# Performance work log

Measured on AMD Instinct MI355X. Metric: run time of the kernel, lower is better.

The kernel has to match this reference:

```python
import jax, jax.numpy as jnp
import numpy as np
import math

DIM = 2048
NUM_HEADS = 16
HEAD_DIM = 128
SEQ = 2048
BATCH = 2
THETA = 10000.0


def _rope_freqs(seq_len, head_dim, theta=THETA):
    half = head_dim // 2
    inv = 1.0 / (theta ** (np.arange(0, half, dtype=np.float32) / half))
    t = np.arange(seq_len, dtype=np.float32)
    ang = np.outer(t, inv)  # [S, half]
    return jnp.asarray(np.cos(ang)), jnp.asarray(np.sin(ang))


def setup_inputs() -> dict:
    key = jax.random.key(0)
    ks = jax.random.split(key, 5)
    s = 1.0 / math.sqrt(DIM)
    cos, sin = _rope_freqs(SEQ, HEAD_DIM)
    return {
        "x": jax.random.normal(ks[0], (BATCH, SEQ, DIM), dtype=jnp.float32),
        "wq": jax.random.normal(ks[1], (DIM, NUM_HEADS * HEAD_DIM), dtype=jnp.float32) * s,
        "wk": jax.random.normal(ks[2], (DIM, NUM_HEADS * HEAD_DIM), dtype=jnp.float32) * s,
        "wv": jax.random.normal(ks[3], (DIM, NUM_HEADS * HEAD_DIM), dtype=jnp.float32) * s,
        "wo": jax.random.normal(ks[4], (NUM_HEADS * HEAD_DIM, DIM), dtype=jnp.float32) * s,
        "freqs_cos": cos,
        "freqs_sin": sin,
    }


def _apply_rope(x, cos, sin):
    # x: [B, S, H, Hd]; cos/sin: [S, Hd//2]
    B, S, H, Hd = x.shape
    xr = x.astype(jnp.float32).reshape(B, S, H, Hd // 2, 2)
    x0, x1 = xr[..., 0], xr[..., 1]
    c = cos[:S][None, :, None, :]
    sn = sin[:S][None, :, None, :]
    o0 = x0 * c - x1 * sn
    o1 = x0 * sn + x1 * c
    return jnp.stack([o0, o1], axis=-1).reshape(B, S, H, Hd)


def reference(x, wq, wk, wv, wo, freqs_cos, freqs_sin):
    B, S, D = x.shape
    H, Hd = NUM_HEADS, HEAD_DIM
    q = (x @ wq).reshape(B, S, H, Hd)
    k = (x @ wk).reshape(B, S, H, Hd)
    v = (x @ wv).reshape(B, S, H, Hd)
    q = _apply_rope(q, freqs_cos, freqs_sin)
    k = _apply_rope(k, freqs_cos, freqs_sin)
    # [B, H, S, S] causal attention scores
    scores = jnp.einsum("bqhd,bkhd->bhqk", q, k) / math.sqrt(Hd)
    causal = jnp.tril(jnp.ones((S, S), dtype=bool))
    scores = jnp.where(causal[None, None], scores, -jnp.inf)
    probs = jax.nn.softmax(scores.astype(jnp.float32), axis=-1)
    o = jnp.einsum("bhqk,bkhd->bqhd", probs, v).reshape(B, S, H * Hd)
    return o @ wo
```

## Files before the change

kernel.cpp:

```cpp
#include <hip/hip_runtime.h>
#include <hip/hip_bf16.h>

typedef __bf16 bf16;
typedef __attribute__((ext_vector_type(8))) __bf16 bf16x8;
typedef __attribute__((ext_vector_type(4))) __bf16 bf16x4;
typedef __attribute__((ext_vector_type(4))) float  f32x4;

typedef const void __attribute__((address_space(1)))* gas_t;
typedef void __attribute__((address_space(3)))* las_t;

__device__ __forceinline__ void gload16(const void* g, void* l) {
  __builtin_amdgcn_global_load_lds((gas_t)g, (las_t)l, 16, 0, 0);
}
__device__ __forceinline__ f32x4 mfma16(bf16x8 a, bf16x8 b, f32x4 c) {
  return __builtin_amdgcn_mfma_f32_16x16x32_bf16(a, b, c, 0, 0, 0);
}

constexpr int SEQL = 2048;
constexpr int DM   = 2048;
constexpr int HD   = 128;
constexpr int MR   = 4096;

__global__ __launch_bounds__(256) void cvt_x(const float* __restrict__ x,
                                             bf16* __restrict__ xb) {
  const size_t i = ((size_t)blockIdx.x * 256 + threadIdx.x) * 4;
  const f32x4 v = *reinterpret_cast<const f32x4*>(x + i);
  bf16x4 o;
  #pragma unroll
  for (int j = 0; j < 4; ++j) o[j] = (bf16)v[j];
  *reinterpret_cast<bf16x4*>(xb + i) = o;
}

__global__ __launch_bounds__(256) void transpose_w(
    const float* __restrict__ w0, const float* __restrict__ w1,
    const float* __restrict__ w2, const float* __restrict__ w3,
    bf16* __restrict__ wqkvt, bf16* __restrict__ wot) {
  const int z = blockIdx.z;
  const float* src = (z == 0) ? w0 : (z == 1) ? w1 : (z == 2) ? w2 : w3;
  bf16* dst = (z < 3) ? (wqkvt + (size_t)z * DM * DM) : wot;
  __shared__ float tile[32][33];
  const int tx = threadIdx.x, ty = threadIdx.y;
  const int x0 = blockIdx.x * 32, y0 = blockIdx.y * 32;
  #pragma unroll
  for (int i = 0; i < 4; ++i)
    tile[ty + 8 * i][tx] = src[(size_t)(y0 + ty + 8 * i) * DM + x0 + tx];
  __syncthreads();
  #pragma unroll
  for (int i = 0; i < 4; ++i)
    dst[(size_t)(x0 + ty + 8 * i) * DM + y0 + tx] = (bf16)tile[tx][ty + 8 * i];
}

__global__ __launch_bounds__(256) void rope_k(bf16* __restrict__ Q,
                                              bf16* __restrict__ Kk,
                                              const float* __restrict__ fc,
                                              const float* __restrict__ fs) {
  bf16* X = blockIdx.y ? Kk : Q;
  const size_t tid = (size_t)blockIdx.x * 256 + threadIdx.x;
  const size_t e0 = tid * 8;
  const int col = (int)(e0 & (DM - 1));
  const int row = (int)(e0 >> 11);
  const int s   = row & (SEQL - 1);
  const int p0  = (col & (HD - 1)) >> 1;
  bf16x8 v = *reinterpret_cast<bf16x8*>(X + e0);
  const f32x4 c  = *reinterpret_cast<const f32x4*>(fc + (size_t)s * 64 + p0);
  const f32x4 sn = *reinterpret_cast<const f32x4*>(fs + (size_t)s * 64 + p0);
  #pragma unroll
  for (int j = 0; j < 4; ++j) {
    const float x0 = (float)v[2 * j], x1 = (float)v[2 * j + 1];
    v[2 * j]     = (bf16)(x0 * c[j] - x1 * sn[j]);
    v[2 * j + 1] = (bf16)(x0 * sn[j] + x1 * c[j]);
  }
  *reinterpret_cast<bf16x8*>(X + e0) = v;
}

template <bool MULTI, bool OUTF32>
__global__ __launch_bounds__(256) void gemm_bt(
    const bf16* __restrict__ A, const bf16* __restrict__ Bt,
    bf16* __restrict__ Cb, float* __restrict__ Cf,
    const int M, const int N, const int K) {
  const int t = threadIdx.x;
  const int wid = t >> 6, lane = t & 63, lo = lane & 15, hi = lane >> 4;
  const int m0 = blockIdx.y * 128, n0 = blockIdx.x * 128;
  const bf16* Bt_ = Bt;
  bf16* Cb_ = Cb;
  if (MULTI) {
    const size_t z = blockIdx.z;
    Bt_ += z * (size_t)N * K;
    Cb_ += z * (size_t)M * N;
  }
  __shared__ bf16 As[128 * 32];
  __shared__ bf16 Bs[128 * 32];
  const int wr = wid >> 1, wc = wid & 1;
  const f32x4 zero4 = {0.f, 0.f, 0.f, 0.f};
  f32x4 acc[4][4];
  #pragma unroll
  for (int i = 0; i < 4; ++i)
    #pragma unroll
    for (int j = 0; j < 4; ++j) acc[i][j] = zero4;

  const int r_a = t >> 2;
  const int ul  = ((t & 3) ^ (r_a & 3)) * 8;
  const bf16* gA0 = A   + (size_t)(m0 + r_a) * K + ul;
  const bf16* gB0 = Bt_ + (size_t)(n0 + r_a) * K + ul;
  char* lA = (char*)As + wid * 1024;
  char* lB = (char*)Bs + wid * 1024;

  const int ru = (hi ^ (lo & 3)) * 8;

  for (int k0 = 0; k0 < K; k0 += 32) {
    gload16(gA0 + k0, lA);
    gload16(gA0 + (size_t)64 * K + k0, lA + 4096);
    gload16(gB0 + k0, lB);
    gload16(gB0 + (size_t)64 * K + k0, lB + 4096);
    __syncthreads();
    bf16x8 af[4], bb[4];
    #pragma unroll
    for (int i = 0; i < 4; ++i)
      af[i] = *reinterpret_cast<const bf16x8*>(As + (wr * 64 + i * 16 + lo) * 32 + ru);
    #pragma unroll
    for (int i = 0; i < 4; ++i)
      bb[i] = *reinterpret_cast<const bf16x8*>(Bs + (wc * 64 + i * 16 + lo) * 32 + ru);
    #pragma unroll
    for (int mi = 0; mi < 4; ++mi)
      #pragma unroll
      for (int ni = 0; ni < 4; ++ni)
        acc[mi][ni] = mfma16(af[mi], bb[ni], acc[mi][ni]);
    __syncthreads();
  }
  #pragma unroll
  for (int mi = 0; mi < 4; ++mi)
    #pragma unroll
    for (int ni = 0; ni < 4; ++ni)
      #pragma unroll
      for (int r = 0; r < 4; ++r) {
        const size_t row = m0 + wr * 64 + mi * 16 + hi * 4 + r;
        const size_t col = n0 + wc * 64 + ni * 16 + lo;
        if (OUTF32) Cf[row * N + col] = acc[mi][ni][r];
        else        Cb_[row * N + col] = (bf16)acc[mi][ni][r];
      }
}

__global__ __launch_bounds__(256) void flash_fwd(
    const bf16* __restrict__ Qg, const bf16* __restrict__ Kg,
    const bf16* __restrict__ Vg, bf16* __restrict__ Og) {
  const int t = threadIdx.x;
  const int wid = t >> 6, lane = t & 63, lo = lane & 15, hi = lane >> 4;
  const int q0 = blockIdx.x * 64;
  const int h  = blockIdx.y;
  const int b  = blockIdx.z;

  __shared__ bf16 Ks[64 * 128];
  __shared__ bf16 Vt[128 * 64];
  __shared__ bf16 Ps[4][16 * 64];

  const size_t hoff = (size_t)b * SEQL * DM + (size_t)h * HD;

  bf16x8 qf[4];
  {
    const bf16* qrow = Qg + hoff + (size_t)(q0 + wid * 16 + lo) * DM;
    #pragma unroll
    for (int kc = 0; kc < 4; ++kc)
      qf[kc] = *reinterpret_cast<const bf16x8*>(qrow + kc * 32 + hi * 8);
  }

  const f32x4 zero4 = {0.f, 0.f, 0.f, 0.f};
  f32x4 acc[8];
  #pragma unroll
  for (int i = 0; i < 8; ++i) acc[i] = zero4;
  float m_r[4], l_r[4];
  #pragma unroll
  for (int r = 0; r < 4; ++r) { m_r[r] = -1e30f; l_r[r] = 0.f; }

  const int ntiles = q0 / 64 + 1;
  const float scale = 0.08838834764831845f;

  const int krow = t >> 4;
  const int kul  = ((t & 15) ^ krow) * 8;
  const int vd0  = (t & 31) * 4;
  const int vg   = t >> 5;

  for (int it = 0; it < ntiles; ++it) {
    const int kv0 = it * 64;
    {
      const bf16* gK = Kg + hoff + (size_t)(kv0 + krow) * DM + kul;
      char* lK = (char*)Ks + wid * 1024;
      #pragma unroll
      for (int j = 0; j < 4; ++j)
        gload16(gK + (size_t)j * 16 * DM, lK + j * 4096);
    }
    {
      const bf16* gV = Vg + hoff + (size_t)kv0 * DM + vd0;
      bf16x4 ld[8];
      #pragma unroll
      for (int e = 0; e < 8; ++e)
        ld[e] = *reinterpret_cast<const bf16x4*>(gV + (size_t)(vg * 8 + e) * DM);
      #pragma unroll
      for (int c = 0; c < 4; ++c) {
        const int d = vd0 + c;
        const int sw = (d ^ (d >> 3)) & 7;
        bf16x8 pk;
        #pragma unroll
        for (int e = 0; e < 8; ++e) pk[e] = ld[e][c];
        *reinterpret_cast<bf16x8*>(Vt + d * 64 + ((vg ^ sw) * 8)) = pk;
      }
    }
    __syncthreads();

    f32x4 s[4];
    #pragma unroll
    for (int nf = 0; nf < 4; ++nf) s[nf] = zero4;
    #pragma unroll
    for (int nf = 0; nf < 4; ++nf) {
      const bf16* krp = Ks + (nf * 16 + lo) * 128;
      #pragma unroll
      for (int kc = 0; kc < 4; ++kc) {
        const bf16x8 kb = *reinterpret_cast<const bf16x8*>(krp + (((kc * 4 + hi) ^ lo) * 8));
        s[nf] = mfma16(qf[kc], kb, s[nf]);
      }
    }
    const bool boundary = (kv0 == q0);
    #pragma unroll
    for (int nf = 0; nf < 4; ++nf)
      #pragma unroll
      for (int r = 0; r < 4; ++r) {
        float v = s[nf][r] * scale;
        if (boundary && (nf * 16 + lo > wid * 16 + hi * 4 + r)) v = -1e30f;
        s[nf][r] = v;
      }
    float fctr[4];
    #pragma unroll
    for (int r = 0; r < 4; ++r) {
      float mx = fmaxf(fmaxf(s[0][r], s[1][r]), fmaxf(s[2][r], s[3][r]));
      #pragma unroll
      for (int msk = 1; msk < 16; msk <<= 1) mx = fmaxf(mx, __shfl_xor(mx, msk, 64));
      const float mnew = fmaxf(m_r[r], mx);
      fctr[r] = __expf(m_r[r] - mnew);
      m_r[r] = mnew;
      float sum = 0.f;
      #pragma unroll
      for (int nf = 0; nf < 4; ++nf) {
        const float p = __expf(s[nf][r] - mnew);
        s[nf][r] = p;
        sum += p;
      }
      l_r[r] = l_r[r] * fctr[r] + sum;
    }
    #pragma unroll
    for (int i = 0; i < 8; ++i)
      #pragma unroll
      for (int r = 0; r < 4; ++r) acc[i][r] *= fctr[r];
    bf16* myP = Ps[wid];
    #pragma unroll
    for (int nf = 0; nf < 4; ++nf)
      #pragma unroll
      for (int r = 0; r < 4; ++r) {
        const int row = hi * 4 + r;
        const int col = nf * 16 + lo;
        myP[row * 64 + (((col >> 3) ^ (row & 7)) * 8) + (col & 7)] = (bf16)s[nf][r];
      }
    bf16x8 pa[2];
    #pragma unroll
    for (int kc = 0; kc < 2; ++kc)
      pa[kc] = *reinterpret_cast<const bf16x8*>(myP + lo * 64 + (((kc * 4 + hi) ^ (lo & 7)) * 8));
    #pragma unroll
    for (int nf = 0; nf < 8; ++nf) {
      const int d = nf * 16 + lo;
      const int sw = (d ^ (d >> 3)) & 7;
      const bf16* vrp = Vt + d * 64;
      #pragma unroll
      for (int kc = 0; kc < 2; ++kc) {
        const bf16x8 bv = *reinterpret_cast<const bf16x8*>(vrp + (((kc * 4 + hi) ^ sw) * 8));
        acc[nf] = mfma16(pa[kc], bv, acc[nf]);
      }
    }
    __syncthreads();
  }

  #pragma unroll
  for (int r = 0; r < 4; ++r) {
    float l = l_r[r];
    #pragma unroll
    for (int msk = 1; msk < 16; msk <<= 1) l += __shfl_xor(l, msk, 64);
    l_r[r] = 1.f / l;
  }
  #pragma unroll
  for (int nf = 0; nf < 8; ++nf)
    #pragma unroll
    for (int r = 0; r < 4; ++r) {
      const size_t row = q0 + wid * 16 + hi * 4 + r;
      Og[hoff + row * DM + nf * 16 + lo] = (bf16)(acc[nf][r] * l_r[r]);
    }
}

extern "C" void kernel_launch(void* const* d_in, const int* in_sizes, int n_in,
                              void* d_out, int out_size, void* d_ws, size_t ws_size,
                              hipStream_t stream) {
  const float* x  = (const float*)d_in[0];
  const float* wq = (const float*)d_in[1];
  const float* wk = (const float*)d_in[2];
  const float* wv = (const float*)d_in[3];
  const float* wo = (const float*)d_in[4];
  const float* fc = (const float*)d_in[5];
  const float* fs = (const float*)d_in[6];
  float* out = (float*)d_out;

  char* ws = (char*)d_ws;
  bf16* xb    = (bf16*)ws;
  bf16* wqkvt = (bf16*)(ws + (16ull << 20));
  bf16* wot   = (bf16*)(ws + (40ull << 20));
  bf16* qkv   = (bf16*)(ws + (48ull << 20));
  bf16* Qb = qkv;
  bf16* Kb = qkv + (size_t)MR * DM;
  bf16* Vb = qkv + 2 * (size_t)MR * DM;

  cvt_x<<<8192, 256, 0, stream>>>(x, xb);
  transpose_w<<<dim3(64, 64, 4), dim3(32, 8), 0, stream>>>(wq, wk, wv, wo, wqkvt, wot);
  gemm_bt<true, false><<<dim3(16, 32, 3), 256, 0, stream>>>(xb, wqkvt, qkv, nullptr, MR, DM, DM);
  rope_k<<<dim3(4096, 2), 256, 0, stream>>>(Qb, Kb, fc, fs);
  flash_fwd<<<dim3(32, 16, 2), 256, 0, stream>>>(Qb, Kb, Vb, xb );
  gemm_bt<false, true><<<dim3(16, 32), 256, 0, stream>>>(xb, wot, nullptr, out, MR, DM, DM);
}
```

Measured before the change: 506.4 us.

## Pair causal query tiles per block and streamline flash-attention softmax

Each flash-attention block now handles two query tiles (i and 31-i), halving the grid so every block does equal causal work. The QK^T MFMA operands are swapped so each lane owns one query row, which turns the row max and sum reductions into two cross-lane shuffles. The softmax uses exp2 with a folded log2 scale and skips rescaling the accumulator when no row max in the wave grows. The P store to shared memory is vectorised. The cost is a grid of 512 blocks instead of 1024, which may lower occupancy and latency hiding on a chip with many CUs.

```diff
diff --git a/kernel.cpp b/kernel.cpp
--- a/kernel.cpp
+++ b/kernel.cpp
@@ -145,7 +145,6 @@
     const bf16* __restrict__ Vg, bf16* __restrict__ Og) {
   const int t = threadIdx.x;
   const int wid = t >> 6, lane = t & 63, lo = lane & 15, hi = lane >> 4;
-  const int q0 = blockIdx.x * 64;
   const int h  = blockIdx.y;
   const int b  = blockIdx.z;
 
@@ -154,142 +153,154 @@
   __shared__ bf16 Ps[4][16 * 64];
 
   const size_t hoff = (size_t)b * SEQL * DM + (size_t)h * HD;
-
-  bf16x8 qf[4];
-  {
-    const bf16* qrow = Qg + hoff + (size_t)(q0 + wid * 16 + lo) * DM;
-    #pragma unroll
-    for (int kc = 0; kc < 4; ++kc)
-      qf[kc] = *reinterpret_cast<const bf16x8*>(qrow + kc * 32 + hi * 8);
-  }
-
-  const f32x4 zero4 = {0.f, 0.f, 0.f, 0.f};
-  f32x4 acc[8];
-  #pragma unroll
-  for (int i = 0; i < 8; ++i) acc[i] = zero4;
-  float m_r[4], l_r[4];
-  #pragma unroll
-  for (int r = 0; r < 4; ++r) { m_r[r] = -1e30f; l_r[r] = 0.f; }
-
-  const int ntiles = q0 / 64 + 1;
-  const float scale = 0.08838834764831845f;
+  const float SCALE_LOG2 = 0.12751743f;
 
   const int krow = t >> 4;
   const int kul  = ((t & 15) ^ krow) * 8;
   const int vd0  = (t & 31) * 4;
   const int vg   = t >> 5;
-
-  for (int it = 0; it < ntiles; ++it) {
-    const int kv0 = it * 64;
+  char* myP = (char*)(Ps[wid]);
+  const f32x4 zero4 = {0.f, 0.f, 0.f, 0.f};
+
+  #pragma unroll 1
+  for (int pass = 0; pass < 2; ++pass) {
+    const int q0 = (pass ? (31 - (int)blockIdx.x) : (int)blockIdx.x) * 64;
+
+    bf16x8 qf[4];
     {
-      const bf16* gK = Kg + hoff + (size_t)(kv0 + krow) * DM + kul;
-      char* lK = (char*)Ks + wid * 1024;
-      #pragma unroll
-      for (int j = 0; j < 4; ++j)
-        gload16(gK + (size_t)j * 16 * DM, lK + j * 4096);
+      const bf16* qrow = Qg + hoff + (size_t)(q0 + wid * 16 + lo) * DM;
+      #pragma unroll
+      for (int kc = 0; kc < 4; ++kc)
+        qf[kc] = *reinterpret_cast<const bf16x8*>(qrow + kc * 32 + hi * 8);
     }
-    {
-      const bf16* gV = Vg + hoff + (size_t)kv0 * DM + vd0;
-      bf16x4 ld[8];
-      #pragma unroll
-      for (int e = 0; e < 8; ++e)
-        ld[e] = *reinterpret_cast<const bf16x4*>(gV + (size_t)(vg * 8 + e) * DM);
-      #pragma unroll
-      for (int c = 0; c < 4; ++c) {
-        const int d = vd0 + c;
+
+    f32x4 acc[8];
+    #pragma unroll
+    for (int i = 0; i < 8; ++i) acc[i] = zero4;
+    float m_run = -1e30f, l_run = 0.f;
+
+    const int ntiles = q0 / 64 + 1;
+    #pragma unroll 1
+    for (int it = 0; it < ntiles; ++it) {
+      const int kv0 = it * 64;
+      {
+        const bf16* gK = Kg + hoff + (size_t)(kv0 + krow) * DM + kul;
+        char* lK = (char*)Ks + wid * 1024;
+        #pragma unroll
+        for (int j = 0; j < 4; ++j)
+          gload16(gK + (size_t)j * 16 * DM, lK + j * 4096);
+      }
+      {
+        const bf16* gV = Vg + hoff + (size_t)kv0 * DM + vd0;
+        bf16x4 ld[8];
+        #pragma unroll
+        for (int e = 0; e < 8; ++e)
+          ld[e] = *reinterpret_cast<const bf16x4*>(gV + (size_t)(vg * 8 + e) * DM);
+        #pragma unroll
+        for (int c = 0; c < 4; ++c) {
+          const int d = vd0 + c;
+          const int sw = (d ^ (d >> 3)) & 7;
+          bf16x8 pk;
+          #pragma unroll
+          for (int e = 0; e < 8; ++e) pk[e] = ld[e][c];
+          *reinterpret_cast<bf16x8*>(Vt + d * 64 + ((vg ^ sw) * 8)) = pk;
+        }
+      }
+      __syncthreads();
+
+      f32x4 s[4];
+      #pragma unroll
+      for (int nf = 0; nf < 4; ++nf) s[nf] = zero4;
+      #pragma unroll
+      for (int nf = 0; nf < 4; ++nf) {
+        const bf16* krp = Ks + (nf * 16 + lo) * 128;
+        #pragma unroll
+        for (int kc = 0; kc < 4; ++kc) {
+          const bf16x8 kb = *reinterpret_cast<const bf16x8*>(krp + (((kc * 4 + hi) ^ lo) * 8));
+          s[nf] = mfma16(kb, qf[kc], s[nf]);
+        }
+      }
+      const bool boundary = (kv0 == q0);
+      #pragma unroll
+      for (int nf = 0; nf < 4; ++nf)
+        #pragma unroll
+        for (int r = 0; r < 4; ++r) {
+          float v = s[nf][r] * SCALE_LOG2;
+          if (boundary && (nf * 16 + hi * 4 + r > wid * 16 + lo)) v = -1e30f;
+          s[nf][r] = v;
+        }
+      float pmax = -1e30f;
+      #pragma unroll
+      for (int nf = 0; nf < 4; ++nf)
+        #pragma unroll
+        for (int r = 0; r < 4; ++r) pmax = fmaxf(pmax, s[nf][r]);
+      pmax = fmaxf(pmax, __shfl_xor(pmax, 16, 64));
+      pmax = fmaxf(pmax, __shfl_xor(pmax, 32, 64));
+      float mnew = m_run;
+      if (!__all(pmax <= m_run)) {
+        mnew = fmaxf(m_run, pmax);
+        const float fctr = exp2f(m_run - mnew);
+        m_run = mnew;
+        l_run *= fctr;
+        float fa[4];
+        #pragma unroll
+        for (int r = 0; r < 4; ++r) fa[r] = __shfl(fctr, hi * 4 + r, 64);
+        #pragma unroll
+        for (int i = 0; i < 8; ++i)
+          #pragma unroll
+          for (int r = 0; r < 4; ++r) acc[i][r] *= fa[r];
+      }
+      float sum = 0.f;
+      #pragma unroll
+      for (int nf = 0; nf < 4; ++nf)
+        #pragma unroll
+        for (int r = 0; r < 4; ++r) {
+          const float p = exp2f(s[nf][r] - mnew);
+          s[nf][r] = p;
+          sum += p;
+        }
+      sum += __shfl_xor(sum, 16, 64);
+      sum += __shfl_xor(sum, 32, 64);
+      l_run += sum;
+      #pragma unroll
+      for (int nf = 0; nf < 4; ++nf) {
+        bf16x4 w;
+        #pragma unroll
+        for (int r = 0; r < 4; ++r) w[r] = (bf16)s[nf][r];
+        *reinterpret_cast<bf16x4*>(myP + lo * 128 +
+            (((nf * 2 + (hi >> 1)) ^ (lo & 7)) * 16) + (hi & 1) * 8) = w;
+      }
+      bf16x8 pa[2];
+      #pragma unroll
+      for (int kc = 0; kc < 2; ++kc)
+        pa[kc] = *reinterpret_cast<const bf16x8*>(myP + lo * 128 +
+            (((kc * 4 + hi) ^ (lo & 7)) * 16));
+      #pragma unroll
+      for (int nf = 0; nf < 8; ++nf) {
+        const int d = nf * 16 + lo;
         const int sw = (d ^ (d >> 3)) & 7;
-        bf16x8 pk;
-        #pragma unroll
-        for (int e = 0; e < 8; ++e) pk[e] = ld[e][c];
-        *reinterpret_cast<bf16x8*>(Vt + d * 64 + ((vg ^ sw) * 8)) = pk;
-      }
+        const bf16* vrp = Vt + d * 64;
+        #pragma unroll
+        for (int kc = 0; kc < 2; ++kc) {
+          const bf16x8 bv = *reinterpret_cast<const bf16x8*>(vrp + (((kc * 4 + hi) ^ sw) * 8));
+          acc[nf] = mfma16(pa[kc], bv, acc[nf]);
+        }
+      }
+      __syncthreads();
     }
-    __syncthreads();
-
-    f32x4 s[4];
-    #pragma unroll
-    for (int nf = 0; nf < 4; ++nf) s[nf] = zero4;
-    #pragma unroll
-    for (int nf = 0; nf < 4; ++nf) {
-      const bf16* krp = Ks + (nf * 16 + lo) * 128;
-      #pragma unroll
-      for (int kc = 0; kc < 4; ++kc) {
-        const bf16x8 kb = *reinterpret_cast<const bf16x8*>(krp + (((kc * 4 + hi) ^ lo) * 8));
-        s[nf] = mfma16(qf[kc], kb, s[nf]);
-      }
-    }
-    const bool boundary = (kv0 == q0);
-    #pragma unroll
-    for (int nf = 0; nf < 4; ++nf)
+
+    const float linv = 1.f / l_run;
+    float la[4];
+    #pragma unroll
+    for (int r = 0; r < 4; ++r) la[r] = __shfl(linv, hi * 4 + r, 64);
+    #pragma unroll
+    for (int nf = 0; nf < 8; ++nf)
       #pragma unroll
       for (int r = 0; r < 4; ++r) {
-        float v = s[nf][r] * scale;
-        if (boundary && (nf * 16 + lo > wid * 16 + hi * 4 + r)) v = -1e30f;
-        s[nf][r] = v;
-      }
-    float fctr[4];
-    #pragma unroll
-    for (int r = 0; r < 4; ++r) {
-      float mx = fmaxf(fmaxf(s[0][r], s[1][r]), fmaxf(s[2][r], s[3][r]));
-      #pragma unroll
-      for (int msk = 1; msk < 16; msk <<= 1) mx = fmaxf(mx, __shfl_xor(mx, msk, 64));
-      const float mnew = fmaxf(m_r[r], mx);
-      fctr[r] = __expf(m_r[r] - mnew);
-      m_r[r] = mnew;
-      float sum = 0.f;
-      #pragma unroll
-      for (int nf = 0; nf < 4; ++nf) {
-        const float p = __expf(s[nf][r] - mnew);
-        s[nf][r] = p;
-        sum += p;
-      }
-      l_r[r] = l_r[r] * fctr[r] + sum;
-    }
-    #pragma unroll
-    for (int i = 0; i < 8; ++i)
-      #pragma unroll
-      for (int r = 0; r < 4; ++r) acc[i][r] *= fctr[r];
-    bf16* myP = Ps[wid];
-    #pragma unroll
-    for (int nf = 0; nf < 4; ++nf)
-      #pragma unroll
-      for (int r = 0; r < 4; ++r) {
-        const int row = hi * 4 + r;
-        const int col = nf * 16 + lo;
-        myP[row * 64 + (((col >> 3) ^ (row & 7)) * 8) + (col & 7)] = (bf16)s[nf][r];
-      }
-    bf16x8 pa[2];
-    #pragma unroll
-    for (int kc = 0; kc < 2; ++kc)
-      pa[kc] = *reinterpret_cast<const bf16x8*>(myP + lo * 64 + (((kc * 4 + hi) ^ (lo & 7)) * 8));
-    #pragma unroll
-    for (int nf = 0; nf < 8; ++nf) {
-      const int d = nf * 16 + lo;
-      const int sw = (d ^ (d >> 3)) & 7;
-      const bf16* vrp = Vt + d * 64;
-      #pragma unroll
-      for (int kc = 0; kc < 2; ++kc) {
-        const bf16x8 bv = *reinterpret_cast<const bf16x8*>(vrp + (((kc * 4 + hi) ^ sw) * 8));
-        acc[nf] = mfma16(pa[kc], bv, acc[nf]);
-      }
-    }
-    __syncthreads();
+        const size_t row = q0 + wid * 16 + hi * 4 + r;
+        Og[hoff + row * DM + nf * 16 + lo] = (bf16)(acc[nf][r] * la[r]);
+      }
   }
-
-  #pragma unroll
-  for (int r = 0; r < 4; ++r) {
-    float l = l_r[r];
-    #pragma unroll
-    for (int msk = 1; msk < 16; msk <<= 1) l += __shfl_xor(l, msk, 64);
-    l_r[r] = 1.f / l;
-  }
-  #pragma unroll
-  for (int nf = 0; nf < 8; ++nf)
-    #pragma unroll
-    for (int r = 0; r < 4; ++r) {
-      const size_t row = q0 + wid * 16 + hi * 4 + r;
-      Og[hoff + row * DM + nf * 16 + lo] = (bf16)(acc[nf][r] * l_r[r]);
-    }
 }
 
 extern "C" void kernel_launch(void* const* d_in, const int* in_sizes, int n_in,
@@ -317,6 +328,6 @@
   transpose_w<<<dim3(64, 64, 4), dim3(32, 8), 0, stream>>>(wq, wk, wv, wo, wqkvt, wot);
   gemm_bt<true, false><<<dim3(16, 32, 3), 256, 0, stream>>>(xb, wqkvt, qkv, nullptr, MR, DM, DM);
   rope_k<<<dim3(4096, 2), 256, 0, stream>>>(Qb, Kb, fc, fs);
-  flash_fwd<<<dim3(32, 16, 2), 256, 0, stream>>>(Qb, Kb, Vb, xb );
+  flash_fwd<<<dim3(16, 16, 2), 256, 0, stream>>>(Qb, Kb, Vb, xb );
   gemm_bt<false, true><<<dim3(16, 32), 256, 0, stream>>>(xb, wot, nullptr, out, MR, DM, DM);
 }
```

Result: faster. 437.9 us (-13.5%).
